# Performance work log

Measured on AMD Instinct MI355X. Metric: run time of the kernel, lower is better.

Reference implementation:

```python
import jax, jax.numpy as jnp
import numpy as np

IN_F, OUT_F = 256, 256
GRID, ORDER = 5, 3
K = GRID + ORDER + 1  # 9 knots
EPS_MINMAX = 1e-7     # K.epsilon()
EPS_BN = 1e-3         # keras BatchNormalization default epsilon


def setup_inputs() -> dict:
    key = jax.random.key(0)
    ks = jax.random.split(key, 4)
    x = jax.random.normal(ks[0], (32, 32, 32, IN_F), dtype=jnp.float32)
    he = lambda k, shape, fan_in: jax.random.normal(k, shape, jnp.float32) * np.sqrt(2.0 / fan_in)
    base_weight = he(ks[1], (IN_F, OUT_F), IN_F)
    spline_weight = he(ks[2], (OUT_F, IN_F, K), IN_F * K)
    spline_scaler = jnp.ones((OUT_F, IN_F), jnp.float32)
    return {
        'x': x,
        'base_weight': base_weight,
        'spline_weight': spline_weight,
        'spline_scaler': spline_scaler,
        'bn_base_gamma': jnp.ones((OUT_F,), jnp.float32),
        'bn_base_beta': jnp.zeros((OUT_F,), jnp.float32),
        'bn_base_mean': jnp.zeros((OUT_F,), jnp.float32),
        'bn_base_var': jnp.ones((OUT_F,), jnp.float32),
        'bn_spline_gamma': jnp.ones((OUT_F,), jnp.float32),
        'bn_spline_beta': jnp.zeros((OUT_F,), jnp.float32),
        'bn_spline_mean': jnp.zeros((OUT_F,), jnp.float32),
        'bn_spline_var': jnp.ones((OUT_F,), jnp.float32),
    }


def _bn(z, gamma, beta, mean, var):
    # Keras BatchNormalization, inference mode (training=False)
    return gamma * (z - mean) * jax.lax.rsqrt(var + EPS_BN) + beta


def reference(x, base_weight, spline_weight, spline_scaler,
              bn_base_gamma, bn_base_beta, bn_base_mean, bn_base_var,
              bn_spline_gamma, bn_spline_beta, bn_spline_mean, bn_spline_var):
    B, H, W, _ = x.shape
    xf = x.reshape(-1, IN_F)  # [N, in]

    # base path: GEMM -> BN -> SiLU
    base = xf @ base_weight
    base = jax.nn.silu(_bn(base, bn_base_gamma, bn_base_beta, bn_base_mean, bn_base_var))

    # min-max normalize per feature over the flattened batch
    x_min = jnp.min(xf, axis=0, keepdims=True)
    x_max = jnp.max(xf, axis=0, keepdims=True)
    xn = (xf - x_min) / (x_max - x_min + EPS_MINMAX)

    # triangle basis: relu(1 - |x - knot|), knots = linspace(-1, 1, K)
    knots = jnp.linspace(-1.0, 1.0, K, dtype=jnp.float32)
    basis = jnp.maximum(0.0, 1.0 - jnp.abs(xn[:, :, None] - knots[None, None, :]))  # [N, in, K]

    # scaled spline weight, flattened GEMM
    w = (spline_weight * spline_scaler[:, :, None]).reshape(OUT_F, IN_F * K)  # [out, in*K]
    spline = basis.reshape(-1, IN_F * K) @ w.T  # [N, out]
    spline = _bn(spline, bn_spline_gamma, bn_spline_beta, bn_spline_mean, bn_spline_var)

    out = base + spline
    return out.reshape(B, H, W, OUT_F)
```

## Files before the change

kernel.cpp:

```cpp
#include <hip/hip_runtime.h>
#include <stdint.h>
#include <stddef.h>

typedef _Float16 h2 __attribute__((ext_vector_type(2)));
typedef _Float16 h8 __attribute__((ext_vector_type(8)));
typedef float f4 __attribute__((ext_vector_type(4)));

union Hfrag { h2 p[4]; h8 v; };

#define WS_PMIN   0
#define WS_PMAX   524288
#define WS_BT     0
#define WS_SMALL  1048576
#define WS_SCALEV (WS_SMALL + 0)
#define WS_BKN    (WS_SMALL + 1024)
#define WS_C0     (WS_SMALL + 3072)
#define WS_BSC    (WS_SMALL + 4096)
#define WS_BSH    (WS_SMALL + 5120)
#define WS_SSC    (WS_SMALL + 6144)
#define WS_SSH    (WS_SMALL + 7168)

__device__ __forceinline__ void gload_lds16(const void* g, void* l) {
  __builtin_amdgcn_global_load_lds(
      (const __attribute__((address_space(1))) void*)g,
      (__attribute__((address_space(3))) void*)l, 16, 0, 0);
}

__global__ __launch_bounds__(256) void kan_minmax(const float* __restrict__ x,
                                                  float* __restrict__ pmin,
                                                  float* __restrict__ pmax) {
  __shared__ f4 smn[4][64], smx[4][64];
  const int b = blockIdx.x, t = threadIdx.x;
  const int fq = t & 63, rg = t >> 6;
  const float* p = x + (size_t)b * 64 * 256 + (size_t)rg * 16 * 256 + fq * 4;
  f4 mn = (f4)(3.402823466e38f), mx = (f4)(-3.402823466e38f);
#pragma unroll
  for (int j = 0; j < 16; ++j) {
    f4 v = *(const f4*)(p + (size_t)j * 256);
    mn = __builtin_elementwise_min(mn, v);
    mx = __builtin_elementwise_max(mx, v);
  }
  smn[rg][fq] = mn; smx[rg][fq] = mx;
  __syncthreads();
  if (rg == 0) {
#pragma unroll
    for (int g = 1; g < 4; ++g) {
      mn = __builtin_elementwise_min(mn, smn[g][fq]);
      mx = __builtin_elementwise_max(mx, smx[g][fq]);
    }
    *(f4*)(pmin + (size_t)b * 256 + fq * 4) = mn;
    *(f4*)(pmax + (size_t)b * 256 + fq * 4) = mx;
  }
}

__global__ __launch_bounds__(256) void kan_finalize(
    const float* __restrict__ pmin, const float* __restrict__ pmax,
    const float* __restrict__ g1, const float* __restrict__ b1,
    const float* __restrict__ m1, const float* __restrict__ v1,
    const float* __restrict__ g2, const float* __restrict__ b2,
    const float* __restrict__ m2, const float* __restrict__ v2,
    float* __restrict__ scalev, _Float16* __restrict__ bkn,
    float* __restrict__ bscv, float* __restrict__ bshv,
    float* __restrict__ sscv, float* __restrict__ sshv) {
  __shared__ f4 smn[256], smx[256];
  const int t = threadIdx.x, q = blockIdx.x;
  const float* pm = pmin + (size_t)t * 256 + q * 4;
  const float* px = pmax + (size_t)t * 256 + q * 4;
  f4 mn = __builtin_elementwise_min(*(const f4*)pm, *(const f4*)(pm + 256 * 256));
  f4 mx = __builtin_elementwise_max(*(const f4*)px, *(const f4*)(px + 256 * 256));
  smn[t] = mn; smx[t] = mx;
  __syncthreads();
  for (int st = 128; st > 0; st >>= 1) {
    if (t < st) {
      smn[t] = __builtin_elementwise_min(smn[t], smn[t + st]);
      smx[t] = __builtin_elementwise_max(smx[t], smx[t + st]);
    }
    __syncthreads();
  }
  if (t == 0) {
    const f4 fmn = smn[0], fmx = smx[0];
#pragma unroll
    for (int j = 0; j < 4; ++j) {
      const int o = q * 4 + j;
      const float mnS = fmn[j], mxS = fmx[j];
      const float rng = mxS - mnS + 1e-7f;
      scalev[o] = 1.0f / rng;
      const float step = 0.25f * rng;
#pragma unroll
      for (int jj = 0; jj < 4; ++jj)
        bkn[jj * 256 + o] = (_Float16)(mnS + step * (float)jj);
      const float bs = g1[o] / sqrtf(v1[o] + 1e-3f);
      bscv[o] = bs;
      bshv[o] = b1[o] - m1[o] * bs;
      const float ss = g2[o] / sqrtf(v2[o] + 1e-3f);
      sscv[o] = ss;
      sshv[o] = b2[o] - m2[o] * ss;
    }
  }
}

__global__ __launch_bounds__(256) void kan_buildw(
    const float* __restrict__ spline_w, const float* __restrict__ spline_s,
    const float* __restrict__ base_w, const float* __restrict__ scalev,
    _Float16* __restrict__ Bt, float* __restrict__ C0) {
  const int og = blockIdx.x;
  const int i  = threadIdx.x;
  const float* wp = spline_w + (size_t)(og * 256 + i) * 9;
  const float w1 = wp[1], w2 = wp[2], w3 = wp[3], w4 = wp[4];
  const float w5 = wp[5], w6 = wp[6], w7 = wp[7], w8 = wp[8];
  const float s  = spline_s[og * 256 + i];
  const float sc = scalev[i];
  const float wp0 = 0.25f*w1 + 0.5f*w2 + 0.75f*w3 + w4 + 0.75f*w5 + 0.5f*w6 + 0.25f*w7;
  float wj[4];
  wj[0] = (w5 + w6 + w7 + w8) - (w1 + w2 + w3 + w4);
  wj[1] = w1 - 2.0f * w5;
  wj[2] = w2 - 2.0f * w6;
  wj[3] = w3 - 2.0f * w7;
  const float ssc = s * sc;
  const int half = og >> 7, o = og & 127, ic = i >> 5, kk = i & 31;
  const size_t base = (size_t)ic * 64000 + (size_t)half * 25600 + (size_t)o * 40 + kk;
#pragma unroll
  for (int j = 0; j < 4; ++j)
    Bt[base + (size_t)j * 5120] = (_Float16)(wj[j] * ssc);
  Bt[base + 4 * 5120] = (_Float16)base_w[(size_t)i * 256 + og];
  __shared__ float red[256];
  red[i] = wp0 * s;
  __syncthreads();
  for (int st = 128; st > 0; st >>= 1) {
    if (i < st) red[i] += red[i + st];
    __syncthreads();
  }
  if (i == 0) C0[og] = red[0];
}

__global__ __launch_bounds__(256, 2) void kan_gemm(
    const float* __restrict__ x, const _Float16* __restrict__ Bt,
    const _Float16* __restrict__ bkn, const float* __restrict__ C0,
    const float* __restrict__ bscv, const float* __restrict__ bshv,
    const float* __restrict__ sscv, const float* __restrict__ sshv,
    float* __restrict__ out) {
  const int tid = threadIdx.x;
  const int lane = tid & 63;
  const int wv = tid >> 6;
  const int wm = wv >> 1, wn = wv & 1;
  const int lr = lane & 15, lg = lane >> 4;
  const int mt = blockIdx.x & 255, nt = blockIdx.x >> 8;

  const int rowA = mt * 128 + wm * 64 + lr;
  const int colB = wn * 64 + lr;

  __shared__ __align__(16) char smem[53248];
  _Float16* sbkn = (_Float16*)(smem + 51200);
  *(uint2*)(sbkn + tid * 4) = ((const uint2*)bkn)[tid];

  f4 accS[4][4], accB[4][4];
#pragma unroll
  for (int m = 0; m < 4; ++m)
#pragma unroll
    for (int n = 0; n < 4; ++n) { accS[m][n] = (f4)0.0f; accB[m][n] = (f4)0.0f; }

  h2 hz; hz[0] = (_Float16)0.0f; hz[1] = (_Float16)0.0f;

  const int rowb = colB * 80 + lg * 16;

  f4 xa[4], xb[4];
  {
    const int ib = lg * 8;
#pragma unroll
    for (int m = 0; m < 4; ++m) {
      const float* px = x + (size_t)(rowA + m * 16) * 256 + ib;
      xa[m] = *(const f4*)px; xb[m] = *(const f4*)(px + 4);
    }
  }

#define LOADB(BF, J)                                                         \
  _Pragma("unroll")                                                          \
  for (int n = 0; n < 4; ++n)                                                \
    BF[n].v = *(const h8*)(smem + rowb + (J) * 10240 + n * 1280);

#define SPLINE_STEP(J, BF)                                                   \
  {                                                                          \
    Hfrag bbj;                                                               \
    bbj.v = *(const h8*)(sbkn + (J) * 256 + ic * 32 + lg * 8);               \
    _Pragma("unroll")                                                        \
    for (int m = 0; m < 4; ++m) {                                            \
      Hfrag afm;                                                             \
      _Pragma("unroll")                                                      \
      for (int qq = 0; qq < 4; ++qq) {                                       \
        h2 d = xh[m].p[qq] - bbj.p[qq];                                      \
        afm.p[qq] = __builtin_elementwise_max(d, hz);                        \
      }                                                                      \
      _Pragma("unroll")                                                      \
      for (int n = 0; n < 4; ++n)                                            \
        accS[m][n] = __builtin_amdgcn_mfma_f32_16x16x32_f16(afm.v, BF[n].v,  \
                                                            accS[m][n], 0, 0, 0); \
    }                                                                        \
  }

#pragma unroll 1
  for (int ic = 0; ic < 8; ++ic) {
    __syncthreads();
    {
      const char* gsrc = (const char*)Bt + (size_t)ic * 128000 + (size_t)nt * 51200;
#pragma unroll
      for (int r = 0; r < 13; ++r) {
        const int idx = r * 256 + tid;
        if (idx < 3200)
          gload_lds16(gsrc + (size_t)idx * 16, smem + r * 4096 + wv * 1024);
      }
    }
    asm volatile("s_waitcnt vmcnt(0)" ::: "memory");
    __syncthreads();

    Hfrag xh[4];
#pragma unroll
    for (int m = 0; m < 4; ++m) {
      xh[m].p[0][0] = (_Float16)xa[m].x; xh[m].p[0][1] = (_Float16)xa[m].y;
      xh[m].p[1][0] = (_Float16)xa[m].z; xh[m].p[1][1] = (_Float16)xa[m].w;
      xh[m].p[2][0] = (_Float16)xb[m].x; xh[m].p[2][1] = (_Float16)xb[m].y;
      xh[m].p[3][0] = (_Float16)xb[m].z; xh[m].p[3][1] = (_Float16)xb[m].w;
    }

    __builtin_amdgcn_sched_barrier(0);
    if (ic < 7) {
      const int ib = (ic + 1) * 32 + lg * 8;
#pragma unroll
      for (int m = 0; m < 4; ++m) {
        const float* px = x + (size_t)(rowA + m * 16) * 256 + ib;
        xa[m] = *(const f4*)px; xb[m] = *(const f4*)(px + 4);
      }
    }
    __builtin_amdgcn_sched_barrier(0);

    Hfrag bfA[4], bfB[4];
    LOADB(bfA, 0)
    LOADB(bfB, 1)
    SPLINE_STEP(0, bfA)
    LOADB(bfA, 2)
    SPLINE_STEP(1, bfB)
    LOADB(bfB, 3)
    SPLINE_STEP(2, bfA)
    LOADB(bfA, 4)
    SPLINE_STEP(3, bfB)

#pragma unroll
    for (int m = 0; m < 4; ++m)
#pragma unroll
      for (int n = 0; n < 4; ++n)
        accB[m][n] = __builtin_amdgcn_mfma_f32_16x16x32_f16(xh[m].v, bfA[n].v, accB[m][n], 0, 0, 0);
  }
#undef SPLINE_STEP
#undef LOADB

#pragma unroll
  for (int n = 0; n < 4; ++n) {
    const int col = nt * 128 + colB + n * 16;
    const float vbs = bscv[col], vbh = bshv[col];
    const float vss = sscv[col];
    const float vsh = sshv[col] + vss * C0[col];
#pragma unroll
    for (int m = 0; m < 4; ++m) {
      const int row0 = mt * 128 + wm * 64 + m * 16 + lg * 4;
#pragma unroll
      for (int r = 0; r < 4; ++r) {
        const float zb = accB[m][n][r] * vbs + vbh;
        const float si = zb / (1.0f + __expf(-zb));
        const float val = si + accS[m][n][r] * vss + vsh;
        out[(size_t)(row0 + r) * 256 + col] = val;
      }
    }
  }
}

extern "C" void kernel_launch(void* const* d_in, const int* in_sizes, int n_in,
                              void* d_out, int out_size, void* d_ws, size_t ws_size,
                              hipStream_t stream) {
  const float* x        = (const float*)d_in[0];
  const float* base_w   = (const float*)d_in[1];
  const float* spline_w = (const float*)d_in[2];
  const float* spline_s = (const float*)d_in[3];
  const float* g1 = (const float*)d_in[4];
  const float* b1 = (const float*)d_in[5];
  const float* m1 = (const float*)d_in[6];
  const float* v1 = (const float*)d_in[7];
  const float* g2 = (const float*)d_in[8];
  const float* b2 = (const float*)d_in[9];
  const float* m2 = (const float*)d_in[10];
  const float* v2 = (const float*)d_in[11];
  float* out = (float*)d_out;
  char* ws = (char*)d_ws;

  float* pmin     = (float*)(ws + WS_PMIN);
  float* pmax     = (float*)(ws + WS_PMAX);
  _Float16* Bt    = (_Float16*)(ws + WS_BT);
  float* scalev   = (float*)(ws + WS_SCALEV);
  _Float16* bkn   = (_Float16*)(ws + WS_BKN);
  float* C0       = (float*)(ws + WS_C0);
  float* bscv     = (float*)(ws + WS_BSC);
  float* bshv     = (float*)(ws + WS_BSH);
  float* sscv     = (float*)(ws + WS_SSC);
  float* sshv     = (float*)(ws + WS_SSH);

  kan_minmax<<<512, 256, 0, stream>>>(x, pmin, pmax);
  kan_finalize<<<64, 256, 0, stream>>>(pmin, pmax, g1, b1, m1, v1, g2, b2, m2, v2,
                                       scalev, bkn, bscv, bshv, sscv, sshv);
  kan_buildw<<<256, 256, 0, stream>>>(spline_w, spline_s, base_w, scalev, Bt, C0);
  kan_gemm<<<512, 256, 0, stream>>>(x, Bt, bkn, C0, bscv, bshv, sscv, sshv, out);
}
```

Before: 143.6 us.

## Shift x by per-feature min so first spline step becomes plain MFMA, relayout B tile

Subtracts the per-feature minimum from x before the fp16 conversion, so the first knot offset is zero and the j=0 spline step reduces to a direct MFMA with no elementwise basis work. The base GEMM's resulting bias is restored through a new per-column correction (Cb) folded into the BN shift. The B tile layout in the workspace changes to a contiguous per-k-group layout that drops the bounds-checked partial staging loop and shrinks LDS. This saves ALU work per tile and may raise occupancy, at the cost of an extra reduction in buildw and some fp16 precision risk from the shifted inputs.

```diff
diff --git a/kernel.cpp b/kernel.cpp
--- a/kernel.cpp
+++ b/kernel.cpp
@@ -14,11 +14,13 @@
 #define WS_SMALL  1048576
 #define WS_SCALEV (WS_SMALL + 0)
 #define WS_BKN    (WS_SMALL + 1024)
-#define WS_C0     (WS_SMALL + 3072)
-#define WS_BSC    (WS_SMALL + 4096)
-#define WS_BSH    (WS_SMALL + 5120)
-#define WS_SSC    (WS_SMALL + 6144)
-#define WS_SSH    (WS_SMALL + 7168)
+#define WS_MINV   (WS_SMALL + 3072)
+#define WS_C0     (WS_SMALL + 4096)
+#define WS_CB     (WS_SMALL + 5120)
+#define WS_BSC    (WS_SMALL + 6144)
+#define WS_BSH    (WS_SMALL + 7168)
+#define WS_SSC    (WS_SMALL + 8192)
+#define WS_SSH    (WS_SMALL + 9216)
 
 __device__ __forceinline__ void gload_lds16(const void* g, void* l) {
   __builtin_amdgcn_global_load_lds(
@@ -60,6 +62,7 @@
     const float* __restrict__ g2, const float* __restrict__ b2,
     const float* __restrict__ m2, const float* __restrict__ v2,
     float* __restrict__ scalev, _Float16* __restrict__ bkn,
+    float* __restrict__ minv,
     float* __restrict__ bscv, float* __restrict__ bshv,
     float* __restrict__ sscv, float* __restrict__ sshv) {
   __shared__ f4 smn[256], smx[256];
@@ -85,10 +88,11 @@
       const float mnS = fmn[j], mxS = fmx[j];
       const float rng = mxS - mnS + 1e-7f;
       scalev[o] = 1.0f / rng;
+      minv[o] = mnS;
       const float step = 0.25f * rng;
 #pragma unroll
-      for (int jj = 0; jj < 4; ++jj)
-        bkn[jj * 256 + o] = (_Float16)(mnS + step * (float)jj);
+      for (int jj = 1; jj < 4; ++jj)
+        bkn[(jj - 1) * 256 + o] = (_Float16)(step * (float)jj);
       const float bs = g1[o] / sqrtf(v1[o] + 1e-3f);
       bscv[o] = bs;
       bshv[o] = b1[o] - m1[o] * bs;
@@ -102,7 +106,8 @@
 __global__ __launch_bounds__(256) void kan_buildw(
     const float* __restrict__ spline_w, const float* __restrict__ spline_s,
     const float* __restrict__ base_w, const float* __restrict__ scalev,
-    _Float16* __restrict__ Bt, float* __restrict__ C0) {
+    const float* __restrict__ minv,
+    _Float16* __restrict__ Bt, float* __restrict__ C0, float* __restrict__ Cb) {
   const int og = blockIdx.x;
   const int i  = threadIdx.x;
   const float* wp = spline_w + (size_t)(og * 256 + i) * 9;
@@ -110,6 +115,7 @@
   const float w5 = wp[5], w6 = wp[6], w7 = wp[7], w8 = wp[8];
   const float s  = spline_s[og * 256 + i];
   const float sc = scalev[i];
+  const float bw = base_w[(size_t)i * 256 + og];
   const float wp0 = 0.25f*w1 + 0.5f*w2 + 0.75f*w3 + w4 + 0.75f*w5 + 0.5f*w6 + 0.25f*w7;
   float wj[4];
   wj[0] = (w5 + w6 + w7 + w8) - (w1 + w2 + w3 + w4);
@@ -118,11 +124,12 @@
   wj[3] = w3 - 2.0f * w7;
   const float ssc = s * sc;
   const int half = og >> 7, o = og & 127, ic = i >> 5, kk = i & 31;
-  const size_t base = (size_t)ic * 64000 + (size_t)half * 25600 + (size_t)o * 40 + kk;
+  const size_t base = (size_t)(ic * 2 + half) * 20480 +
+                      (size_t)(kk >> 3) * 1024 + (size_t)o * 8 + (kk & 7);
 #pragma unroll
   for (int j = 0; j < 4; ++j)
-    Bt[base + (size_t)j * 5120] = (_Float16)(wj[j] * ssc);
-  Bt[base + 4 * 5120] = (_Float16)base_w[(size_t)i * 256 + og];
+    Bt[base + (size_t)j * 4096] = (_Float16)(wj[j] * ssc);
+  Bt[base + 4 * 4096] = (_Float16)bw;
   __shared__ float red[256];
   red[i] = wp0 * s;
   __syncthreads();
@@ -131,11 +138,20 @@
     __syncthreads();
   }
   if (i == 0) C0[og] = red[0];
+  __syncthreads();
+  red[i] = minv[i] * bw;
+  __syncthreads();
+  for (int st = 128; st > 0; st >>= 1) {
+    if (i < st) red[i] += red[i + st];
+    __syncthreads();
+  }
+  if (i == 0) Cb[og] = red[0];
 }
 
 __global__ __launch_bounds__(256, 2) void kan_gemm(
     const float* __restrict__ x, const _Float16* __restrict__ Bt,
-    const _Float16* __restrict__ bkn, const float* __restrict__ C0,
+    const _Float16* __restrict__ bkn, const float* __restrict__ minv,
+    const float* __restrict__ C0, const float* __restrict__ Cb,
     const float* __restrict__ bscv, const float* __restrict__ bshv,
     const float* __restrict__ sscv, const float* __restrict__ sshv,
     float* __restrict__ out) {
@@ -149,9 +165,11 @@
   const int rowA = mt * 128 + wm * 64 + lr;
   const int colB = wn * 64 + lr;
 
-  __shared__ __align__(16) char smem[53248];
-  _Float16* sbkn = (_Float16*)(smem + 51200);
-  *(uint2*)(sbkn + tid * 4) = ((const uint2*)bkn)[tid];
+  __shared__ __align__(16) char smem[43520];
+  float* smnf = (float*)(smem + 40960);
+  _Float16* sdb = (_Float16*)(smem + 41984);
+  smnf[tid] = minv[tid];
+  if (tid < 192) ((uint2*)sdb)[tid] = ((const uint2*)bkn)[tid];
 
   f4 accS[4][4], accB[4][4];
 #pragma unroll
@@ -161,27 +179,23 @@
 
   h2 hz; hz[0] = (_Float16)0.0f; hz[1] = (_Float16)0.0f;
 
-  const int rowb = colB * 80 + lg * 16;
-
-  f4 xa[4], xb[4];
-  {
-    const int ib = lg * 8;
-#pragma unroll
-    for (int m = 0; m < 4; ++m) {
-      const float* px = x + (size_t)(rowA + m * 16) * 256 + ib;
-      xa[m] = *(const f4*)px; xb[m] = *(const f4*)(px + 4);
-    }
+#define STAGE(IC)                                                            \
+  {                                                                          \
+    const char* gs = (const char*)Bt + (size_t)((IC) * 2 + nt) * 40960;      \
+    _Pragma("unroll")                                                        \
+    for (int r = 0; r < 10; ++r)                                             \
+      gload_lds16(gs + (size_t)(r * 256 + tid) * 16, smem + r * 4096 + wv * 1024); \
   }
 
 #define LOADB(BF, J)                                                         \
   _Pragma("unroll")                                                          \
   for (int n = 0; n < 4; ++n)                                                \
-    BF[n].v = *(const h8*)(smem + rowb + (J) * 10240 + n * 1280);
+    BF[n].v = *(const h8*)(smem + (J) * 8192 + lg * 2048 + colB * 16 + n * 256);
 
 #define SPLINE_STEP(J, BF)                                                   \
   {                                                                          \
     Hfrag bbj;                                                               \
-    bbj.v = *(const h8*)(sbkn + (J) * 256 + ic * 32 + lg * 8);               \
+    bbj.v = *(const h8*)(sdb + ((J) - 1) * 256 + ic * 32 + lg * 8);          \
     _Pragma("unroll")                                                        \
     for (int m = 0; m < 4; ++m) {                                            \
       Hfrag afm;                                                             \
@@ -197,28 +211,33 @@
     }                                                                        \
   }
 
+  f4 xa[4], xb[4];
+  {
+    const int ib = lg * 8;
+#pragma unroll
+    for (int m = 0; m < 4; ++m) {
+      const float* px = x + (size_t)(rowA + m * 16) * 256 + ib;
+      xa[m] = *(const f4*)px; xb[m] = *(const f4*)(px + 4);
+    }
+  }
+
 #pragma unroll 1
   for (int ic = 0; ic < 8; ++ic) {
     __syncthreads();
-    {
-      const char* gsrc = (const char*)Bt + (size_t)ic * 128000 + (size_t)nt * 51200;
-#pragma unroll
-      for (int r = 0; r < 13; ++r) {
-        const int idx = r * 256 + tid;
-        if (idx < 3200)
-          gload_lds16(gsrc + (size_t)idx * 16, smem + r * 4096 + wv * 1024);
-      }
-    }
+    STAGE(ic)
     asm volatile("s_waitcnt vmcnt(0)" ::: "memory");
     __syncthreads();
 
+    const f4* smn4 = (const f4*)smnf;
+    const f4 mn0 = smn4[ic * 8 + lg * 2], mn1 = smn4[ic * 8 + lg * 2 + 1];
     Hfrag xh[4];
 #pragma unroll
     for (int m = 0; m < 4; ++m) {
-      xh[m].p[0][0] = (_Float16)xa[m].x; xh[m].p[0][1] = (_Float16)xa[m].y;
-      xh[m].p[1][0] = (_Float16)xa[m].z; xh[m].p[1][1] = (_Float16)xa[m].w;
-      xh[m].p[2][0] = (_Float16)xb[m].x; xh[m].p[2][1] = (_Float16)xb[m].y;
-      xh[m].p[3][0] = (_Float16)xb[m].z; xh[m].p[3][1] = (_Float16)xb[m].w;
+      f4 na = xa[m] - mn0, nb = xb[m] - mn1;
+      xh[m].p[0][0] = (_Float16)na.x; xh[m].p[0][1] = (_Float16)na.y;
+      xh[m].p[1][0] = (_Float16)na.z; xh[m].p[1][1] = (_Float16)na.w;
+      xh[m].p[2][0] = (_Float16)nb.x; xh[m].p[2][1] = (_Float16)nb.y;
+      xh[m].p[3][0] = (_Float16)nb.z; xh[m].p[3][1] = (_Float16)nb.w;
     }
 
     __builtin_amdgcn_sched_barrier(0);
@@ -235,14 +254,17 @@
     Hfrag bfA[4], bfB[4];
     LOADB(bfA, 0)
     LOADB(bfB, 1)
-    SPLINE_STEP(0, bfA)
+#pragma unroll
+    for (int m = 0; m < 4; ++m)
+#pragma unroll
+      for (int n = 0; n < 4; ++n)
+        accS[m][n] = __builtin_amdgcn_mfma_f32_16x16x32_f16(xh[m].v, bfA[n].v, accS[m][n], 0, 0, 0);
     LOADB(bfA, 2)
     SPLINE_STEP(1, bfB)
     LOADB(bfB, 3)
     SPLINE_STEP(2, bfA)
     LOADB(bfA, 4)
     SPLINE_STEP(3, bfB)
-
 #pragma unroll
     for (int m = 0; m < 4; ++m)
 #pragma unroll
@@ -251,11 +273,12 @@
   }
 #undef SPLINE_STEP
 #undef LOADB
+#undef STAGE
 
 #pragma unroll
   for (int n = 0; n < 4; ++n) {
     const int col = nt * 128 + colB + n * 16;
-    const float vbs = bscv[col], vbh = bshv[col];
+    const float vbs = bscv[col], vbh = bshv[col] + vbs * Cb[col];
     const float vss = sscv[col];
     const float vsh = sshv[col] + vss * C0[col];
 #pragma unroll
@@ -295,7 +318,9 @@
   _Float16* Bt    = (_Float16*)(ws + WS_BT);
   float* scalev   = (float*)(ws + WS_SCALEV);
   _Float16* bkn   = (_Float16*)(ws + WS_BKN);
+  float* minv     = (float*)(ws + WS_MINV);
   float* C0       = (float*)(ws + WS_C0);
+  float* Cb       = (float*)(ws + WS_CB);
   float* bscv     = (float*)(ws + WS_BSC);
   float* bshv     = (float*)(ws + WS_BSH);
   float* sscv     = (float*)(ws + WS_SSC);
@@ -303,7 +328,9 @@
 
   kan_minmax<<<512, 256, 0, stream>>>(x, pmin, pmax);
   kan_finalize<<<64, 256, 0, stream>>>(pmin, pmax, g1, b1, m1, v1, g2, b2, m2, v2,
-                                       scalev, bkn, bscv, bshv, sscv, sshv);
-  kan_buildw<<<256, 256, 0, stream>>>(spline_w, spline_s, base_w, scalev, Bt, C0);
-  kan_gemm<<<512, 256, 0, stream>>>(x, Bt, bkn, C0, bscv, bshv, sscv, sshv, out);
-}
+                                       scalev, bkn, minv, bscv, bshv, sscv, sshv);
+  kan_buildw<<<256, 256, 0, stream>>>(spline_w, spline_s, base_w, scalev, minv,
+                                      Bt, C0, Cb);
+  kan_gemm<<<512, 256, 0, stream>>>(x, Bt, bkn, minv, C0, Cb,
+                                    bscv, bshv, sscv, sshv, out);
+}
```

Result: no change. 143.1 us (-0.4%).
